# Kernel tuning notes

Hardware: AMD Instinct MI355X
Metric: run time of the kernel (lower is better)

## Reference

```python
import jax, jax.numpy as jnp
import numpy as np

L, B, D = 48, 32, 128  # seq_len, n_bottom_tokens, hidden_dim


def setup_inputs() -> dict:
    key = jax.random.key(0)
    ks = jax.random.split(key, 6)
    s = 0.05
    return {
        "x_embedding": jax.random.normal(ks[0], (L, D), jnp.float32),
        "W_leaf": jax.random.normal(ks[1], (D, 2 * D), jnp.float32) * s,
        "b_leaf": jnp.zeros((2 * D,), jnp.float32),
        "W_tree": jax.random.normal(ks[2], (2 * D, 5 * D), jnp.float32) * s,
        "b_tree": jnp.zeros((5 * D,), jnp.float32),
        "W_a1": jax.random.normal(ks[3], (2 * D, D), jnp.float32) * s,
        "b_a1": jnp.zeros((D,), jnp.float32),
        "W_a2": jax.random.normal(ks[4], (D, 1), jnp.float32) * s,
        "b_a2": jnp.zeros((1,), jnp.float32),
        "bottom_idx": jnp.arange(B, dtype=jnp.int32),
    }


def _forward(x_embedding, W_leaf, b_leaf, W_tree, b_tree, W_a1, b_a1, W_a2, b_a2, bottom_idx):
    # leaf transformation: linear -> split into (h, c), then gather bottom tokens
    hc = x_embedding @ W_leaf + b_leaf
    h_all, c_all = jnp.split(hc, 2, axis=-1)
    hidden = h_all[bottom_idx]  # (B, D)
    cell = c_all[bottom_idx]    # (B, D)
    Bn, Dn = hidden.shape
    mask0 = jnp.ones((Bn,), hidden.dtype)      # 1 = dep still unassigned
    eye = jnp.eye(Bn, dtype=hidden.dtype)
    NEG = jnp.asarray(-1e9, hidden.dtype)

    def step(carry, _):
        hidden, cell, mask = carry
        # all (head, dep) pair features: (B, B, 2D)
        feats = jnp.concatenate([
            jnp.broadcast_to(hidden[:, None, :], (Bn, Bn, Dn)),
            jnp.broadcast_to(hidden[None, :, :], (Bn, Bn, Dn))], axis=-1)
        # binary tree-LSTM cell on every pair
        gates = feats @ W_tree + b_tree  # (B, B, 5D)
        i, fl, fr, g, o = jnp.split(gates, 5, axis=-1)
        c_new = (jax.nn.sigmoid(i) * jnp.tanh(g)
                 + jax.nn.sigmoid(fl) * cell[:, None, :]
                 + jax.nn.sigmoid(fr) * cell[None, :, :])
        h_new = jax.nn.sigmoid(o) * jnp.tanh(c_new)  # (B, B, D)
        # arc scorer MLP -> (B, B)
        score = (jax.nn.relu(feats @ W_a1 + b_a1) @ W_a2 + b_a2)[..., 0]
        # valid arcs: off-diagonal, dep column still unassigned
        arc_mask = (1.0 - eye) * mask[None, :]
        flat_mask = arc_mask.ravel()
        logits = jnp.where(flat_mask > 0, score.ravel(), NEG)
        logp = jax.nn.log_softmax(logits)
        p = jnp.exp(logp)
        # eval-mode deterministic action: argmax over valid probs
        idx = jnp.argmax(jnp.where(flat_mask > 0, p, 0.0))
        a2d = jax.nn.one_hot(idx, Bn * Bn, dtype=hidden.dtype).reshape(Bn, Bn)
        head_oh = a2d.sum(axis=1)  # one-hot over heads
        dep_oh = a2d.sum(axis=0)   # one-hot over deps
        sel_h = jnp.einsum('hd,hdk->hk', a2d, h_new)  # only head row nonzero
        sel_c = jnp.einsum('hd,hdk->hk', a2d, c_new)
        um = head_oh[:, None]
        hidden = hidden * (1.0 - um) + sel_h
        cell = cell * (1.0 - um) + sel_c
        mask = mask * (1.0 - dep_oh)
        lp = logp[idx]
        n_valid = flat_mask.sum()
        ent = -jnp.sum(jnp.where(flat_mask > 0, p * logp, 0.0)) / jnp.log(n_valid)
        return (hidden, cell, mask), (lp, ent, idx // Bn, jnp.mod(idx, Bn))

    (hidden, cell, mask), (lps, ents, heads, deps) = jax.lax.scan(
        step, (hidden, cell, mask0), None, length=Bn - 1)
    edges = jnp.stack([bottom_idx[heads], bottom_idx[deps]], axis=-1)  # (B-1, 2)
    return hidden, jnp.sum(lps), jnp.mean(ents), edges


def reference(x_embedding, W_leaf, b_leaf, W_tree, b_tree, W_a1, b_a1, W_a2, b_a2, bottom_idx):
    return _forward(x_embedding, W_leaf, b_leaf, W_tree, b_tree,
                    W_a1, b_a1, W_a2, b_a2, bottom_idx)
```

## Files before the change

### kernel.cpp

```cpp
#include <hip/hip_runtime.h>
#include <math.h>

#define BN 32
#define DN 128
#define NSTEP 31
#define NT 1024

__device__ __forceinline__ float sigf(float x) { return 1.0f / (1.0f + expf(-x)); }

__global__ __launch_bounds__(NT)
void hrl_kernel(const float* __restrict__ x_emb,
                const float* __restrict__ W_leaf,
                const float* __restrict__ b_leaf,
                const float* __restrict__ W_tree,
                const float* __restrict__ b_tree,
                const float* __restrict__ W_a1,
                const float* __restrict__ b_a1,
                const float* __restrict__ W_a2,
                const float* __restrict__ b_a2,
                const int*   __restrict__ bidx,
                float* __restrict__ out)
{
    __shared__ float sh_hidden[BN][DN];
    __shared__ float sh_cell[BN][DN];
    __shared__ float sh_uT[DN][BN];
    __shared__ float sh_vT[DN][BN];
    __shared__ float sh_score[BN][BN];
    __shared__ float sh_g[5*DN];
    __shared__ float sh_w2[DN];
    __shared__ float sh_b1[DN];
    __shared__ float sh_mask[BN];
    __shared__ int   sh_bidx[BN];
    __shared__ float red_a[NT/64], red_b[NT/64];
    __shared__ int   red_i[NT/64];
    __shared__ float sh_maxv;
    __shared__ int   sh_head, sh_dep;
    __shared__ float sh_b2;

    const int tid  = threadIdx.x;
    const int lane = tid & 63;
    const int wid  = tid >> 6;

    if (tid < DN) { sh_w2[tid] = W_a2[tid]; sh_b1[tid] = b_a1[tid]; }
    if (tid < BN) { sh_mask[tid] = 1.0f; sh_bidx[tid] = bidx[tid]; }
    if (tid == 0) sh_b2 = b_a2[0];
    __syncthreads();

    for (int w = tid; w < BN * 2 * DN; w += NT) {
        const int i = w >> 8;
        const int c = w & 255;
        const float* xr = x_emb + sh_bidx[i] * DN;
        float acc = b_leaf[c];
        #pragma unroll 8
        for (int j = 0; j < DN; ++j) acc = fmaf(xr[j], W_leaf[j * 256 + c], acc);
        if (c < DN) sh_hidden[i][c] = acc; else sh_cell[i][c - DN] = acc;
    }
    __syncthreads();

    for (int w = tid; w < BN * 2 * DN; w += NT) {
        const int h = w >> 8;
        const int c = w & 255;
        const int k = c & 127;
        const float* Wp = W_a1 + (c >= DN ? DN * DN : 0) + k;
        float acc = 0.0f;
        #pragma unroll 8
        for (int j = 0; j < DN; ++j) acc = fmaf(sh_hidden[h][j], Wp[j * DN], acc);
        if (c < DN) sh_uT[k][h] = acc; else sh_vT[k][h] = acc;
    }
    __syncthreads();

    {
        const int h = tid >> 5, d = tid & 31;
        float acc = sh_b2;
        #pragma unroll 4
        for (int k = 0; k < DN; ++k) {
            const float pre = sh_uT[k][h] + sh_vT[k][d] + sh_b1[k];
            acc = fmaf(sh_w2[k], fmaxf(pre, 0.0f), acc);
        }
        sh_score[h][d] = acc;
    }
    __syncthreads();

    float lps_sum = 0.0f, ents_sum = 0.0f;

    for (int t = 0; t < NSTEP; ++t) {
        const int h = tid >> 5, d = tid & 31;
        const bool valid = (h != d) && (sh_mask[d] > 0.0f);
        const float s = valid ? sh_score[h][d] : -3.0e38f;

        float m = s;
        #pragma unroll
        for (int off = 32; off > 0; off >>= 1) m = fmaxf(m, __shfl_down(m, off));
        if (lane == 0) red_a[wid] = m;
        __syncthreads();
        if (tid == 0) {
            float mm = red_a[0];
            for (int i = 1; i < NT / 64; ++i) mm = fmaxf(mm, red_a[i]);
            sh_maxv = mm;
        }
        __syncthreads();
        const float maxv = sh_maxv;

        float e = 0.0f, s1 = 0.0f;
        int cand = 0x7fffffff;
        if (valid) {
            const float x = s - maxv;
            const float ex = expf(x);
            e = ex; s1 = ex * x;
            if (s == maxv) cand = tid;
        }
        #pragma unroll
        for (int off = 32; off > 0; off >>= 1) {
            e    += __shfl_down(e, off);
            s1   += __shfl_down(s1, off);
            cand  = min(cand, __shfl_down(cand, off));
        }
        if (lane == 0) { red_a[wid] = e; red_b[wid] = s1; red_i[wid] = cand; }
        __syncthreads();
        if (tid == 0) {
            float E = 0.0f, S1 = 0.0f; int idx = 0x7fffffff;
            for (int i = 0; i < NT / 64; ++i) {
                E += red_a[i]; S1 += red_b[i]; idx = min(idx, red_i[i]);
            }
            const float logE = logf(E);
            const int hh = idx >> 5, dd = idx & 31;
            lps_sum += (sh_score[hh][dd] - maxv) - logE;
            const float nv = (float)((BN - t) * (BN - 1));
            ents_sum += -(S1 / E - logE) / logf(nv);
            sh_head = hh; sh_dep = dd;
            sh_mask[dd] = 0.0f;
            out[BN * DN + 2 + 2 * t]     = (float)sh_bidx[hh];
            out[BN * DN + 2 + 2 * t + 1] = (float)sh_bidx[dd];
        }
        __syncthreads();
        const int head = sh_head, dep = sh_dep;

        if (tid < 5 * DN) {
            const int j = tid;
            const float* Wh = W_tree + j;
            const float* Wd = W_tree + DN * 5 * DN + j;
            float acc = b_tree[j];
            #pragma unroll 8
            for (int k = 0; k < DN; ++k) {
                acc = fmaf(sh_hidden[head][k], Wh[k * 640], acc);
                acc = fmaf(sh_hidden[dep][k],  Wd[k * 640], acc);
            }
            sh_g[j] = acc;
        }
        __syncthreads();

        if (tid < DN) {
            const int k = tid;
            const float ig = sigf(sh_g[k]);
            const float fl = sigf(sh_g[DN + k]);
            const float fr = sigf(sh_g[2 * DN + k]);
            const float gg = tanhf(sh_g[3 * DN + k]);
            const float og = sigf(sh_g[4 * DN + k]);
            const float c  = ig * gg + fl * sh_cell[head][k] + fr * sh_cell[dep][k];
            sh_cell[head][k]   = c;
            sh_hidden[head][k] = og * tanhf(c);
        }
        __syncthreads();

        if (tid < 2 * DN) {
            const int k = tid & 127;
            const float* Wp = W_a1 + (tid >= DN ? DN * DN : 0) + k;
            float acc = 0.0f;
            #pragma unroll 8
            for (int j = 0; j < DN; ++j) acc = fmaf(sh_hidden[head][j], Wp[j * DN], acc);
            if (tid < DN) sh_uT[k][head] = acc; else sh_vT[k][head] = acc;
        }
        __syncthreads();

        if (tid < 2 * BN) {
            const int hh = (tid < BN) ? head : (tid - BN);
            const int dd = (tid < BN) ? tid  : head;
            if (hh != dd) {
                float acc = sh_b2;
                #pragma unroll 4
                for (int k = 0; k < DN; ++k) {
                    const float pre = sh_uT[k][hh] + sh_vT[k][dd] + sh_b1[k];
                    acc = fmaf(sh_w2[k], fmaxf(pre, 0.0f), acc);
                }
                sh_score[hh][dd] = acc;
            }
        }
        __syncthreads();
    }

    for (int w = tid; w < BN * DN; w += NT) out[w] = sh_hidden[w >> 7][w & 127];
    if (tid == 0) {
        out[BN * DN]     = lps_sum;
        out[BN * DN + 1] = ents_sum / (float)NSTEP;
    }
}

extern "C" void kernel_launch(void* const* d_in, const int* in_sizes, int n_in,
                              void* d_out, int out_size, void* d_ws, size_t ws_size,
                              hipStream_t stream) {
    const float* x_emb  = (const float*)d_in[0];
    const float* W_leaf = (const float*)d_in[1];
    const float* b_leaf = (const float*)d_in[2];
    const float* W_tree = (const float*)d_in[3];
    const float* b_tree = (const float*)d_in[4];
    const float* W_a1   = (const float*)d_in[5];
    const float* b_a1   = (const float*)d_in[6];
    const float* W_a2   = (const float*)d_in[7];
    const float* b_a2   = (const float*)d_in[8];
    const int*   bidx   = (const int*)d_in[9];
    float* out = (float*)d_out;

    hipLaunchKernelGGL(hrl_kernel, dim3(1), dim3(NT), 0, stream,
                       x_emb, W_leaf, b_leaf, W_tree, b_tree,
                       W_a1, b_a1, W_a2, b_a2, bidx, out);
}
```

Baseline: 570.2 us.

## Precompute per-row tree gate projections and overlap their update with arc selection

Splits the work into three kernels. The first two run the leaf projection, the initial per-token W_tree half-products (Gh/Gd) and the arc-scorer projections in parallel across many blocks. The persistent kernel replaces the per-step 256x640 gate matvec with a lookup of the cached head and dep projections. The updated head row's projection is refreshed on spare waves while wave 0 does a single-wave softmax/argmax with a bitmask. The score update is spread across all threads with a shuffle reduction, and shared arrays are padded. This removes the serial gate matvec and several barriers per step, at the cost of extra launches and global-memory round trips through the workspace for Gh/Gd.

```diff
diff --git a/kernel.cpp b/kernel.cpp
--- a/kernel.cpp
+++ b/kernel.cpp
@@ -3,159 +3,207 @@
 
 #define BN 32
 #define DN 128
+#define GW 640
 #define NSTEP 31
 #define NT 1024
 
 __device__ __forceinline__ float sigf(float x) { return 1.0f / (1.0f + expf(-x)); }
 
+__global__ __launch_bounds__(256)
+void leaf_kernel(const float* __restrict__ x_emb, const float* __restrict__ W_leaf,
+                 const float* __restrict__ b_leaf, const int* __restrict__ bidx,
+                 float* __restrict__ hidden0, float* __restrict__ cell0)
+{
+    const int i = blockIdx.x;
+    const int c = threadIdx.x;
+    const float* xr = x_emb + bidx[i] * DN;
+    float acc = b_leaf[c];
+    #pragma unroll 16
+    for (int j = 0; j < DN; ++j) acc = fmaf(xr[j], W_leaf[j * 256 + c], acc);
+    if (c < DN) hidden0[i * DN + c] = acc;
+    else        cell0[i * DN + (c - DN)] = acc;
+}
+
+__global__ __launch_bounds__(256)
+void init2_kernel(const float* __restrict__ W_tree, const float* __restrict__ W_a1,
+                  const float* __restrict__ hidden0,
+                  float* __restrict__ Gh, float* __restrict__ Gd,
+                  float* __restrict__ uT0, float* __restrict__ vT0)
+{
+    __shared__ float sh_h[BN][DN + 1];
+    for (int i = threadIdx.x; i < BN * DN; i += 256)
+        sh_h[i >> 7][i & 127] = hidden0[i];
+    __syncthreads();
+    const int task = blockIdx.x * 256 + threadIdx.x;
+    float acc[8];
+    #pragma unroll
+    for (int r = 0; r < 8; ++r) acc[r] = 0.0f;
+    if (task < 5120) {
+        const int rg = task & 3, r0 = rg * 8;
+        const int cc = task >> 2;
+        const int c  = (cc < GW) ? cc : cc - GW;
+        const float* Wt = W_tree + ((cc < GW) ? 0 : DN * GW) + c;
+        #pragma unroll 8
+        for (int k = 0; k < DN; ++k) {
+            const float w = Wt[k * GW];
+            #pragma unroll
+            for (int r = 0; r < 8; ++r) acc[r] = fmaf(sh_h[r0 + r][k], w, acc[r]);
+        }
+        float* Gt = ((cc < GW) ? Gh : Gd) + c;
+        #pragma unroll
+        for (int r = 0; r < 8; ++r) Gt[(r0 + r) * GW] = acc[r];
+    } else if (task < 6144) {
+        const int tt = task - 5120;
+        const int rg = tt & 3, r0 = rg * 8;
+        const int cc = tt >> 2;
+        const int k  = cc & 127;
+        const float* Wp = W_a1 + ((cc < DN) ? 0 : DN * DN) + k;
+        #pragma unroll 8
+        for (int j = 0; j < DN; ++j) {
+            const float w = Wp[j * DN];
+            #pragma unroll
+            for (int r = 0; r < 8; ++r) acc[r] = fmaf(sh_h[r0 + r][j], w, acc[r]);
+        }
+        float* dst = ((cc < DN) ? uT0 : vT0) + k * BN + r0;
+        #pragma unroll
+        for (int r = 0; r < 8; ++r) dst[r] = acc[r];
+    }
+}
+
 __global__ __launch_bounds__(NT)
-void hrl_kernel(const float* __restrict__ x_emb,
-                const float* __restrict__ W_leaf,
-                const float* __restrict__ b_leaf,
-                const float* __restrict__ W_tree,
-                const float* __restrict__ b_tree,
-                const float* __restrict__ W_a1,
-                const float* __restrict__ b_a1,
-                const float* __restrict__ W_a2,
-                const float* __restrict__ b_a2,
-                const int*   __restrict__ bidx,
-                float* __restrict__ out)
+void main_kernel(const float* __restrict__ W_tree, const float* __restrict__ b_tree,
+                 const float* __restrict__ W_a1, const float* __restrict__ b_a1,
+                 const float* __restrict__ W_a2, const float* __restrict__ b_a2,
+                 const int* __restrict__ bidx,
+                 const float* __restrict__ hidden0, const float* __restrict__ cell0,
+                 const float* __restrict__ uT0, const float* __restrict__ vT0,
+                 float* Gh, float* Gd,
+                 float* __restrict__ out)
 {
-    __shared__ float sh_hidden[BN][DN];
-    __shared__ float sh_cell[BN][DN];
-    __shared__ float sh_uT[DN][BN];
-    __shared__ float sh_vT[DN][BN];
-    __shared__ float sh_score[BN][BN];
-    __shared__ float sh_g[5*DN];
-    __shared__ float sh_w2[DN];
-    __shared__ float sh_b1[DN];
-    __shared__ float sh_mask[BN];
+    __shared__ float sh_hidden[BN][DN + 1];
+    __shared__ float sh_cell[BN][DN + 1];
+    __shared__ float sh_uT[DN][BN + 1];
+    __shared__ float sh_vT[DN][BN + 1];
+    __shared__ float sh_score[BN * BN];
+    __shared__ float sh_btree[GW];
+    __shared__ float sh_w2[DN], sh_b1[DN];
     __shared__ int   sh_bidx[BN];
-    __shared__ float red_a[NT/64], red_b[NT/64];
-    __shared__ int   red_i[NT/64];
-    __shared__ float sh_maxv;
-    __shared__ int   sh_head, sh_dep;
+    __shared__ unsigned sh_maskbits;
+    __shared__ int sh_head, sh_dep;
     __shared__ float sh_b2;
 
     const int tid  = threadIdx.x;
     const int lane = tid & 63;
     const int wid  = tid >> 6;
 
+    for (int i = tid; i < BN * DN; i += NT) {
+        sh_hidden[i >> 7][i & 127] = hidden0[i];
+        sh_cell[i >> 7][i & 127]   = cell0[i];
+        sh_uT[i >> 5][i & 31] = uT0[i];
+        sh_vT[i >> 5][i & 31] = vT0[i];
+    }
+    for (int i = tid; i < GW; i += NT) sh_btree[i] = b_tree[i];
     if (tid < DN) { sh_w2[tid] = W_a2[tid]; sh_b1[tid] = b_a1[tid]; }
-    if (tid < BN) { sh_mask[tid] = 1.0f; sh_bidx[tid] = bidx[tid]; }
-    if (tid == 0) sh_b2 = b_a2[0];
+    if (tid < BN) sh_bidx[tid] = bidx[tid];
+    if (tid == 0) { sh_b2 = b_a2[0]; sh_maskbits = 0xFFFFFFFFu; }
     __syncthreads();
 
-    for (int w = tid; w < BN * 2 * DN; w += NT) {
-        const int i = w >> 8;
-        const int c = w & 255;
-        const float* xr = x_emb + sh_bidx[i] * DN;
-        float acc = b_leaf[c];
-        #pragma unroll 8
-        for (int j = 0; j < DN; ++j) acc = fmaf(xr[j], W_leaf[j * 256 + c], acc);
-        if (c < DN) sh_hidden[i][c] = acc; else sh_cell[i][c - DN] = acc;
-    }
-    __syncthreads();
-
-    for (int w = tid; w < BN * 2 * DN; w += NT) {
-        const int h = w >> 8;
-        const int c = w & 255;
-        const int k = c & 127;
-        const float* Wp = W_a1 + (c >= DN ? DN * DN : 0) + k;
-        float acc = 0.0f;
-        #pragma unroll 8
-        for (int j = 0; j < DN; ++j) acc = fmaf(sh_hidden[h][j], Wp[j * DN], acc);
-        if (c < DN) sh_uT[k][h] = acc; else sh_vT[k][h] = acc;
-    }
-    __syncthreads();
+    const int f_o = tid >> 4, f_sub = tid & 15;
+    float w2r[8], b1r[8];
+    #pragma unroll
+    for (int i = 0; i < 8; ++i) { w2r[i] = sh_w2[f_sub * 8 + i]; b1r[i] = sh_b1[f_sub * 8 + i]; }
 
     {
         const int h = tid >> 5, d = tid & 31;
         float acc = sh_b2;
-        #pragma unroll 4
+        #pragma unroll 8
         for (int k = 0; k < DN; ++k) {
             const float pre = sh_uT[k][h] + sh_vT[k][d] + sh_b1[k];
             acc = fmaf(sh_w2[k], fmaxf(pre, 0.0f), acc);
         }
-        sh_score[h][d] = acc;
+        sh_score[h * BN + d] = acc;
     }
     __syncthreads();
 
     float lps_sum = 0.0f, ents_sum = 0.0f;
+    int prev_head = -1;
 
     for (int t = 0; t < NSTEP; ++t) {
-        const int h = tid >> 5, d = tid & 31;
-        const bool valid = (h != d) && (sh_mask[d] > 0.0f);
-        const float s = valid ? sh_score[h][d] : -3.0e38f;
-
-        float m = s;
-        #pragma unroll
-        for (int off = 32; off > 0; off >>= 1) m = fmaxf(m, __shfl_down(m, off));
-        if (lane == 0) red_a[wid] = m;
-        __syncthreads();
-        if (tid == 0) {
-            float mm = red_a[0];
-            for (int i = 1; i < NT / 64; ++i) mm = fmaxf(mm, red_a[i]);
-            sh_maxv = mm;
-        }
-        __syncthreads();
-        const float maxv = sh_maxv;
-
-        float e = 0.0f, s1 = 0.0f;
-        int cand = 0x7fffffff;
-        if (valid) {
-            const float x = s - maxv;
-            const float ex = expf(x);
-            e = ex; s1 = ex * x;
-            if (s == maxv) cand = tid;
-        }
-        #pragma unroll
-        for (int off = 32; off > 0; off >>= 1) {
-            e    += __shfl_down(e, off);
-            s1   += __shfl_down(s1, off);
-            cand  = min(cand, __shfl_down(cand, off));
-        }
-        if (lane == 0) { red_a[wid] = e; red_b[wid] = s1; red_i[wid] = cand; }
-        __syncthreads();
-        if (tid == 0) {
-            float E = 0.0f, S1 = 0.0f; int idx = 0x7fffffff;
-            for (int i = 0; i < NT / 64; ++i) {
-                E += red_a[i]; S1 += red_b[i]; idx = min(idx, red_i[i]);
-            }
-            const float logE = logf(E);
-            const int hh = idx >> 5, dd = idx & 31;
-            lps_sum += (sh_score[hh][dd] - maxv) - logE;
-            const float nv = (float)((BN - t) * (BN - 1));
-            ents_sum += -(S1 / E - logE) / logf(nv);
-            sh_head = hh; sh_dep = dd;
-            sh_mask[dd] = 0.0f;
-            out[BN * DN + 2 + 2 * t]     = (float)sh_bidx[hh];
-            out[BN * DN + 2 + 2 * t + 1] = (float)sh_bidx[dd];
-        }
-        __syncthreads();
+        if (wid == 0) {
+            const unsigned mbits = sh_maskbits;
+            float s_[16]; bool v_[16];
+            float m = -3.0e38f;
+            #pragma unroll
+            for (int i = 0; i < 16; ++i) {
+                const int flat = i * 64 + lane;
+                const int h = flat >> 5, d = flat & 31;
+                const float sc = sh_score[flat];
+                const bool vv = (h != d) && ((mbits >> d) & 1u);
+                s_[i] = sc; v_[i] = vv;
+                m = vv ? fmaxf(m, sc) : m;
+            }
+            #pragma unroll
+            for (int off = 1; off < 64; off <<= 1) m = fmaxf(m, __shfl_xor(m, off));
+            float e = 0.0f, s1 = 0.0f; int cand = 0x7fffffff;
+            #pragma unroll
+            for (int i = 0; i < 16; ++i) {
+                if (v_[i]) {
+                    const float x = s_[i] - m;
+                    const float ex = expf(x);
+                    e += ex; s1 += ex * x;
+                    if (s_[i] == m) cand = min(cand, i * 64 + lane);
+                }
+            }
+            #pragma unroll
+            for (int off = 1; off < 64; off <<= 1) {
+                e    += __shfl_xor(e, off);
+                s1   += __shfl_xor(s1, off);
+                cand  = min(cand, __shfl_xor(cand, off));
+            }
+            const float logE = logf(e);
+            lps_sum -= logE;
+            ents_sum -= (s1 / e - logE) / logf((float)((BN - t) * (BN - 1)));
+            if (lane == 0) {
+                const int hh = cand >> 5, dd = cand & 31;
+                sh_head = hh; sh_dep = dd;
+                sh_maskbits = mbits & ~(1u << dd);
+                out[BN * DN + 2 + 2 * t]     = (float)sh_bidx[hh];
+                out[BN * DN + 2 + 2 * t + 1] = (float)sh_bidx[dd];
+            }
+        } else if (prev_head >= 0) {
+            const float* hrow = sh_hidden[prev_head];
+            const int task = tid - 64;
+            if (task < GW) {
+                const int cc  = task * 2;
+                const int col = (cc < GW) ? cc : cc - GW;
+                const float2* Wt2 = (const float2*)(W_tree + ((cc < GW) ? 0 : DN * GW) + col);
+                float ax = 0.0f, ay = 0.0f;
+                #pragma unroll 16
+                for (int k = 0; k < DN; ++k) {
+                    const float2 w = Wt2[k * (GW / 2)];
+                    const float hv = hrow[k];
+                    ax = fmaf(hv, w.x, ax);
+                    ay = fmaf(hv, w.y, ay);
+                }
+                float* Gt = ((cc < GW) ? Gh : Gd) + prev_head * GW + col;
+                Gt[0] = ax; Gt[1] = ay;
+            }
+        }
+        __syncthreads();
+
         const int head = sh_head, dep = sh_dep;
-
-        if (tid < 5 * DN) {
-            const int j = tid;
-            const float* Wh = W_tree + j;
-            const float* Wd = W_tree + DN * 5 * DN + j;
-            float acc = b_tree[j];
-            #pragma unroll 8
-            for (int k = 0; k < DN; ++k) {
-                acc = fmaf(sh_hidden[head][k], Wh[k * 640], acc);
-                acc = fmaf(sh_hidden[dep][k],  Wd[k * 640], acc);
-            }
-            sh_g[j] = acc;
-        }
-        __syncthreads();
 
         if (tid < DN) {
             const int k = tid;
-            const float ig = sigf(sh_g[k]);
-            const float fl = sigf(sh_g[DN + k]);
-            const float fr = sigf(sh_g[2 * DN + k]);
-            const float gg = tanhf(sh_g[3 * DN + k]);
-            const float og = sigf(sh_g[4 * DN + k]);
+            const float* gh = Gh + head * GW + k;
+            const float* gd = Gd + dep  * GW + k;
+            const float z0 = gh[0]      + gd[0]      + sh_btree[k];
+            const float z1 = gh[DN]     + gd[DN]     + sh_btree[DN + k];
+            const float z2 = gh[2 * DN] + gd[2 * DN] + sh_btree[2 * DN + k];
+            const float z3 = gh[3 * DN] + gd[3 * DN] + sh_btree[3 * DN + k];
+            const float z4 = gh[4 * DN] + gd[4 * DN] + sh_btree[4 * DN + k];
+            const float ig = sigf(z0), fl = sigf(z1), fr = sigf(z2), og = sigf(z4);
+            const float gg = tanhf(z3);
             const float c  = ig * gg + fl * sh_cell[head][k] + fr * sh_cell[dep][k];
             sh_cell[head][k]   = c;
             sh_hidden[head][k] = og * tanhf(c);
@@ -164,28 +212,32 @@
 
         if (tid < 2 * DN) {
             const int k = tid & 127;
-            const float* Wp = W_a1 + (tid >= DN ? DN * DN : 0) + k;
+            const float* Wp = W_a1 + ((tid < DN) ? 0 : DN * DN) + k;
+            const float* hrow = sh_hidden[head];
             float acc = 0.0f;
-            #pragma unroll 8
-            for (int j = 0; j < DN; ++j) acc = fmaf(sh_hidden[head][j], Wp[j * DN], acc);
+            #pragma unroll 32
+            for (int j = 0; j < DN; ++j) acc = fmaf(hrow[j], Wp[j * DN], acc);
             if (tid < DN) sh_uT[k][head] = acc; else sh_vT[k][head] = acc;
         }
         __syncthreads();
 
-        if (tid < 2 * BN) {
-            const int hh = (tid < BN) ? head : (tid - BN);
-            const int dd = (tid < BN) ? tid  : head;
-            if (hh != dd) {
-                float acc = sh_b2;
-                #pragma unroll 4
-                for (int k = 0; k < DN; ++k) {
-                    const float pre = sh_uT[k][hh] + sh_vT[k][dd] + sh_b1[k];
-                    acc = fmaf(sh_w2[k], fmaxf(pre, 0.0f), acc);
-                }
-                sh_score[hh][dd] = acc;
-            }
-        }
-        __syncthreads();
+        {
+            const int hh = (f_o < BN) ? head : (f_o - BN);
+            const int dd = (f_o < BN) ? f_o : head;
+            float p = 0.0f;
+            #pragma unroll
+            for (int i = 0; i < 8; ++i) {
+                const int k = f_sub * 8 + i;
+                const float pre = sh_uT[k][hh] + sh_vT[k][dd] + b1r[i];
+                p = fmaf(w2r[i], fmaxf(pre, 0.0f), p);
+            }
+            #pragma unroll
+            for (int off = 8; off > 0; off >>= 1) p += __shfl_down(p, off, 16);
+            if (f_sub == 0 && hh != dd) sh_score[hh * BN + dd] = p + sh_b2;
+        }
+        __syncthreads();
+
+        prev_head = head;
     }
 
     for (int w = tid; w < BN * DN; w += NT) out[w] = sh_hidden[w >> 7][w & 127];
@@ -210,7 +262,19 @@
     const int*   bidx   = (const int*)d_in[9];
     float* out = (float*)d_out;
 
-    hipLaunchKernelGGL(hrl_kernel, dim3(1), dim3(NT), 0, stream,
-                       x_emb, W_leaf, b_leaf, W_tree, b_tree,
-                       W_a1, b_a1, W_a2, b_a2, bidx, out);
-}
+    float* ws      = (float*)d_ws;
+    float* hidden0 = ws;
+    float* cell0   = ws + 4096;
+    float* uT0     = ws + 8192;
+    float* vT0     = ws + 12288;
+    float* Gh      = ws + 16384;
+    float* Gd      = Gh + BN * GW;
+
+    hipLaunchKernelGGL(leaf_kernel, dim3(BN), dim3(256), 0, stream,
+                       x_emb, W_leaf, b_leaf, bidx, hidden0, cell0);
+    hipLaunchKernelGGL(init2_kernel, dim3(24), dim3(256), 0, stream,
+                       W_tree, W_a1, hidden0, Gh, Gd, uT0, vT0);
+    hipLaunchKernelGGL(main_kernel, dim3(1), dim3(NT), 0, stream,
+                       W_tree, b_tree, W_a1, b_a1, W_a2, b_a2, bidx,
+                       hidden0, cell0, uT0, vT0, Gh, Gd, out);
+}
```

Measured after the change: 798.2 us. 40.0% more time.
